# Kernel optimization log

Hardware: AMD Instinct MI355X
Metric: run time of the kernel (lower is better)

Reference implementation:

```python
import jax, jax.numpy as jnp
import numpy as np

N_NODES = 200000
N_EDGES = 6400000
IN_FEAT = 128
HIDDEN = 16


def gcn_conv(x, W, b, row, col, n):
    # PyG GCNConv: h = X W ; out_i = sum_{(j->i)} d_j^{-1/2} d_i^{-1/2} h_j + b
    # (row = source j, col = target i; self-loops already included in row/col)
    deg = jax.ops.segment_sum(jnp.ones_like(col, dtype=x.dtype), col, num_segments=n)
    dinv = jnp.where(deg > 0, jax.lax.rsqrt(deg), jnp.zeros_like(deg))
    norm = dinv[row] * dinv[col]            # [E+N]
    h = x @ W                               # [N, out] small GEMM
    msg = norm[:, None] * h[row]            # gather over edges
    out = jax.ops.segment_sum(msg, col, num_segments=n)  # scatter-add to targets
    return out + b


def setup_inputs() -> dict:
    key = jax.random.key(0)
    k1, k2, k3, k4 = jax.random.split(key, 4)
    x = jax.random.normal(k1, (N_NODES, IN_FEAT), dtype=jnp.float32)
    edge_index = jax.random.randint(k2, (2, N_EDGES), 0, N_NODES, dtype=jnp.int32)
    # Glorot-ish init for the two linear layers
    W1 = jax.random.normal(k3, (IN_FEAT, HIDDEN), dtype=jnp.float32) / np.sqrt(IN_FEAT)
    W2 = jax.random.normal(k4, (HIDDEN, 1), dtype=jnp.float32) / np.sqrt(HIDDEN)
    b1 = jnp.zeros((HIDDEN,), dtype=jnp.float32)
    b2 = jnp.zeros((1,), dtype=jnp.float32)
    return {"x": x, "edge_index": edge_index, "W1": W1, "b1": b1, "W2": W2, "b2": b2}


def reference(x, edge_index, W1, b1, W2, b2):
    n = x.shape[0]
    # add self-loops (as PyG GCNConv does by default)
    loop = jnp.arange(n, dtype=edge_index.dtype)
    row = jnp.concatenate([edge_index[0], loop])
    col = jnp.concatenate([edge_index[1], loop])
    h = gcn_conv(x, W1, b1, row, col, n)    # [N, 16]
    h = jax.nn.relu(h)
    out = gcn_conv(h, W2, b2, row, col, n)  # [N, 1]
    return out.squeeze(-1)                  # [N]
```

## Files before the change

kernel.cpp:

```cpp
#include <hip/hip_runtime.h>
#include <hip/hip_fp16.h>

#define N_NODES 200000
#define N_EDGES 6400000
#define IN_FEAT 128
#define HIDDEN  16

#define RN 128
#define NRF 1568
#define NC 98
#define CSHIFT 11
#define NPAD (NRF * RN)
#define SRC_MASK 0x3FFFFu
#define SB1 8192
#define SB2 8192
#define BPB 9
#define CAP 5120

typedef float v4f __attribute__((ext_vector_type(4)));
typedef _Float16 f16x8 __attribute__((ext_vector_type(8)));
typedef float f32x4 __attribute__((ext_vector_type(4)));


__global__ __launch_bounds__(256) void k_fcnt(const int* __restrict__ col,
                                              unsigned* __restrict__ fcnt) {
    __shared__ unsigned c[NRF];
    for (int i = threadIdx.x; i < NRF; i += 256) c[i] = 0u;
    __syncthreads();
    const int EPB = N_EDGES / 512;
    const int4* c4 = (const int4*)(col + (size_t)blockIdx.x * EPB);
    for (int i = threadIdx.x; i < EPB / 4; i += 256) {
        int4 v = c4[i];
        atomicAdd(&c[(unsigned)v.x >> 7], 1u);
        atomicAdd(&c[(unsigned)v.y >> 7], 1u);
        atomicAdd(&c[(unsigned)v.z >> 7], 1u);
        atomicAdd(&c[(unsigned)v.w >> 7], 1u);
    }
    __syncthreads();
    for (int i = threadIdx.x; i < NRF; i += 256)
        if (c[i]) atomicAdd(&fcnt[i], c[i]);
}


__global__ __launch_bounds__(1024) void k_scanr(const unsigned* __restrict__ fcnt,
                                                unsigned* __restrict__ foffs,
                                                unsigned* __restrict__ fcur,
                                                unsigned* __restrict__ coffs,
                                                unsigned* __restrict__ ccur) {
    __shared__ unsigned s[1024];
    const int t = threadIdx.x;
    unsigned c0 = (2 * t     < NRF) ? fcnt[2 * t]     : 0u;
    unsigned c1 = (2 * t + 1 < NRF) ? fcnt[2 * t + 1] : 0u;
    unsigned pairsum = c0 + c1;
    s[t] = pairsum;
    __syncthreads();
    #pragma unroll
    for (int d = 1; d < 1024; d <<= 1) {
        unsigned add = (t >= d) ? s[t - d] : 0u;
        __syncthreads();
        s[t] += add;
        __syncthreads();
    }
    unsigned excl = s[t] - pairsum;
    if (2 * t < NRF)     { foffs[2 * t]     = excl;      fcur[2 * t]     = excl; }
    if (2 * t + 1 < NRF) { foffs[2 * t + 1] = excl + c0; fcur[2 * t + 1] = excl + c0; }
    if (t == 1023) foffs[NRF] = s[t];
    __syncthreads();
    if (t < NC)  { unsigned v = foffs[16 * t]; coffs[t] = v; ccur[t] = v; }
    if (t == NC) coffs[NC] = N_EDGES;
}


__global__ __launch_bounds__(256) void k_cscat(const int* __restrict__ row,
                                               const int* __restrict__ col,
                                               unsigned* __restrict__ ccur,
                                               unsigned* __restrict__ tmp1) {
    __shared__ unsigned cnt[NC], gbase[NC], lcur[NC];
    const long long e0 = (long long)blockIdx.x * SB1;
    long long rem = (long long)N_EDGES - e0;
    const int n = rem > SB1 ? SB1 : (int)rem;
    if (threadIdx.x < NC) { cnt[threadIdx.x] = 0u; lcur[threadIdx.x] = 0u; }
    __syncthreads();
    const int4* c4 = (const int4*)(col + e0);
    for (int i = threadIdx.x; i < n / 4; i += 256) {
        int4 v = c4[i];
        atomicAdd(&cnt[(unsigned)v.x >> CSHIFT], 1u);
        atomicAdd(&cnt[(unsigned)v.y >> CSHIFT], 1u);
        atomicAdd(&cnt[(unsigned)v.z >> CSHIFT], 1u);
        atomicAdd(&cnt[(unsigned)v.w >> CSHIFT], 1u);
    }
    __syncthreads();
    if (threadIdx.x < NC)
        gbase[threadIdx.x] = cnt[threadIdx.x] ? atomicAdd(&ccur[threadIdx.x], cnt[threadIdx.x]) : 0u;
    __syncthreads();
    for (int i = threadIdx.x; i < n; i += 256) {
        unsigned c = (unsigned)col[e0 + i];
        unsigned s = (unsigned)row[e0 + i];
        unsigned b = c >> CSHIFT;
        unsigned pos = gbase[b] + atomicAdd(&lcur[b], 1u);
        tmp1[pos] = ((c & 2047u) << 18) | s;
    }
}


__global__ __launch_bounds__(256) void k_fscat(const unsigned* __restrict__ tmp1,
                                               const unsigned* __restrict__ coffs,
                                               unsigned* __restrict__ fcur,
                                               unsigned* __restrict__ tmp2) {
    __shared__ unsigned cnt[16], gbase[16], lcur[16];
    const int b = blockIdx.x / BPB;
    const int sl = blockIdx.x % BPB;
    const unsigned blo = coffs[b], bhi = coffs[b + 1];
    const unsigned lo = blo + (unsigned)sl * SB2;
    if (lo >= bhi) return;
    const unsigned hi = (lo + SB2 < bhi) ? lo + SB2 : bhi;
    const unsigned n = hi - lo;
    if (threadIdx.x < 16) { cnt[threadIdx.x] = 0u; lcur[threadIdx.x] = 0u; }
    __syncthreads();
    for (unsigned i = threadIdx.x; i < n; i += 256)
        atomicAdd(&cnt[tmp1[lo + i] >> 25], 1u);
    __syncthreads();
    if (threadIdx.x < 16)
        gbase[threadIdx.x] = cnt[threadIdx.x]
            ? atomicAdd(&fcur[16 * b + threadIdx.x], cnt[threadIdx.x]) : 0u;
    __syncthreads();
    for (unsigned i = threadIdx.x; i < n; i += 256) {
        unsigned p = tmp1[lo + i];
        unsigned f = p >> 25;
        unsigned pos = gbase[f] + atomicAdd(&lcur[f], 1u);
        tmp2[pos] = p & 0x01FFFFFFu;
    }
}


__global__ __launch_bounds__(256) void k_bsort(const unsigned* __restrict__ tmp,
                                               const unsigned* __restrict__ boffs_r,
                                               unsigned* __restrict__ boffs_n,
                                               float* __restrict__ dinv,
                                               unsigned* __restrict__ sorted) {
    __shared__ unsigned ebuf[CAP];
    __shared__ unsigned obuf[CAP];
    __shared__ unsigned dcnt[RN], dcur[RN], sscan[RN];
    const int r = blockIdx.x;
    const unsigned lo = boffs_r[r], hi = boffs_r[r + 1];
    const unsigned cnt = hi - lo;
    const unsigned node0 = (unsigned)r * RN;
    if (threadIdx.x < RN) dcnt[threadIdx.x] = 0u;
    __syncthreads();

    const bool fits = (cnt <= CAP);
    if (fits) {
        for (unsigned i = threadIdx.x; i < cnt; i += 256) {
            unsigned p = tmp[lo + i];
            ebuf[i] = p;
            atomicAdd(&dcnt[p >> 18], 1u);
        }
    } else {
        for (unsigned i = threadIdx.x; i < cnt; i += 256)
            atomicAdd(&dcnt[tmp[lo + i] >> 18], 1u);
    }
    __syncthreads();

    unsigned c = 0;
    if (threadIdx.x < RN) { c = dcnt[threadIdx.x]; sscan[threadIdx.x] = c; }
    __syncthreads();
    #pragma unroll
    for (int d = 1; d < RN; d <<= 1) {
        unsigned add = 0;
        if (threadIdx.x < RN && threadIdx.x >= d) add = sscan[threadIdx.x - d];
        __syncthreads();
        if (threadIdx.x < RN) sscan[threadIdx.x] += add;
        __syncthreads();
    }
    if (threadIdx.x < RN) {
        unsigned excl = sscan[threadIdx.x] - c;
        dcur[threadIdx.x] = excl;
        unsigned node = node0 + threadIdx.x;
        boffs_n[node] = lo + excl;
        if (node < N_NODES) dinv[node] = rsqrtf((float)c + 1.0f);
    }
    if (r == NRF - 1 && threadIdx.x == 0) boffs_n[NPAD] = hi;
    __syncthreads();

    if (fits) {
        for (unsigned i = threadIdx.x; i < cnt; i += 256) {
            unsigned p = ebuf[i];
            unsigned pos = atomicAdd(&dcur[p >> 18], 1u);
            obuf[pos] = p & SRC_MASK;
        }
        __syncthreads();
        for (unsigned i = threadIdx.x; i < cnt; i += 256)
            sorted[lo + i] = obuf[i];
    } else {
        for (unsigned i = threadIdx.x; i < cnt; i += 256) {
            unsigned p = tmp[lo + i];
            unsigned pos = atomicAdd(&dcur[p >> 18], 1u);
            sorted[lo + pos] = p & SRC_MASK;
        }
    }
}


__global__ __launch_bounds__(256) void k_gemm1(const float* __restrict__ x,
                                               const float* __restrict__ W1,
                                               const float* __restrict__ dinv,
                                               __half* __restrict__ h16) {
    const int wave = (blockIdx.x * 256 + threadIdx.x) >> 6;
    const int lane = threadIdx.x & 63;
    const int m16 = lane & 15;
    const int quad = lane >> 4;
    if (wave * 16 >= N_NODES) return;

    f16x8 bf[4];
    #pragma unroll
    for (int kb = 0; kb < 4; ++kb)
        #pragma unroll
        for (int j = 0; j < 8; ++j)
            bf[kb][j] = (_Float16)W1[(kb * 32 + quad * 8 + j) * HIDDEN + m16];

    const int node0 = wave * 16;
    const float* xrow = x + (size_t)(node0 + m16) * IN_FEAT + quad * 8;
    f32x4 acc = {0.f, 0.f, 0.f, 0.f};
    #pragma unroll
    for (int kb = 0; kb < 4; ++kb) {
        const v4f* p = (const v4f*)(xrow + kb * 32);
        v4f u0 = p[0], u1 = p[1];
        f16x8 af;
        af[0] = (_Float16)u0.x; af[1] = (_Float16)u0.y;
        af[2] = (_Float16)u0.z; af[3] = (_Float16)u0.w;
        af[4] = (_Float16)u1.x; af[5] = (_Float16)u1.y;
        af[6] = (_Float16)u1.z; af[7] = (_Float16)u1.w;
        acc = __builtin_amdgcn_mfma_f32_16x16x32_f16(af, bf[kb], acc, 0, 0, 0);
    }
    #pragma unroll
    for (int r = 0; r < 4; ++r) {
        int node = node0 + quad * 4 + r;
        h16[(size_t)node * HIDDEN + m16] = __float2half(dinv[node] * acc[r]);
    }
}


__global__ __launch_bounds__(256) void k_agg1(const unsigned* __restrict__ sorted,
                                              const unsigned* __restrict__ boffs,
                                              const unsigned* __restrict__ h16u,
                                              const float* __restrict__ dinv,
                                              const float* __restrict__ b1,
                                              const float* __restrict__ W2,
                                              float* __restrict__ tp) {
    const unsigned tid = blockIdx.x * 256 + threadIdx.x;
    const unsigned node = tid >> 3;
    const int l = tid & 7;
    if (node >= N_NODES) return;

    unsigned e = boffs[node];
    const unsigned o1 = boffs[node + 1];
    float ax = 0.f, ay = 0.f;

    unsigned n0 = 0, n1 = 0, n2 = 0, n3 = 0;
    bool have = (e + 4 <= o1);
    if (have) { n0 = sorted[e]; n1 = sorted[e + 1]; n2 = sorted[e + 2]; n3 = sorted[e + 3]; }
    while (have) {
        unsigned c0 = n0, c1 = n1, c2 = n2, c3 = n3;
        e += 4;
        have = (e + 4 <= o1);
        if (have) { n0 = sorted[e]; n1 = sorted[e + 1]; n2 = sorted[e + 2]; n3 = sorted[e + 3]; }
        unsigned v0 = h16u[(size_t)c0 * 8 + l];
        unsigned v1 = h16u[(size_t)c1 * 8 + l];
        unsigned v2 = h16u[(size_t)c2 * 8 + l];
        unsigned v3 = h16u[(size_t)c3 * 8 + l];
        float2 f0 = __half22float2(*(const __half2*)&v0);
        float2 f1 = __half22float2(*(const __half2*)&v1);
        float2 f2 = __half22float2(*(const __half2*)&v2);
        float2 f3 = __half22float2(*(const __half2*)&v3);
        ax += f0.x + f1.x; ay += f0.y + f1.y;
        ax += f2.x + f3.x; ay += f2.y + f3.y;
    }
    for (; e < o1; ++e) {
        unsigned s = sorted[e];
        unsigned v = h16u[(size_t)s * 8 + l];
        float2 f = __half22float2(*(const __half2*)&v);
        ax += f.x; ay += f.y;
    }

    unsigned vs = h16u[(size_t)node * 8 + l];
    float2 fs = __half22float2(*(const __half2*)&vs);
    float di = dinv[node];
    float px = fmaf(di, ax + fs.x, b1[2 * l]);
    float py = fmaf(di, ay + fs.y, b1[2 * l + 1]);
    float r = fmaxf(px, 0.f) * W2[2 * l] + fmaxf(py, 0.f) * W2[2 * l + 1];
    r += __shfl_xor(r, 4, 8);
    r += __shfl_xor(r, 2, 8);
    r += __shfl_xor(r, 1, 8);
    if (l == 0) tp[node] = di * r;
}


__global__ __launch_bounds__(256) void k_agg2(const unsigned* __restrict__ sorted,
                                              const unsigned* __restrict__ boffs,
                                              const float* __restrict__ tp,
                                              const float* __restrict__ dinv,
                                              const float* __restrict__ b2,
                                              float* __restrict__ out) {
    const unsigned node = blockIdx.x * 256 + threadIdx.x;
    if (node >= N_NODES) return;

    unsigned e = boffs[node];
    const unsigned o1 = boffs[node + 1];
    float acc = 0.f;

    unsigned n0 = 0, n1 = 0, n2 = 0, n3 = 0;
    bool have = (e + 4 <= o1);
    if (have) { n0 = sorted[e]; n1 = sorted[e + 1]; n2 = sorted[e + 2]; n3 = sorted[e + 3]; }
    while (have) {
        unsigned c0 = n0, c1 = n1, c2 = n2, c3 = n3;
        e += 4;
        have = (e + 4 <= o1);
        if (have) { n0 = sorted[e]; n1 = sorted[e + 1]; n2 = sorted[e + 2]; n3 = sorted[e + 3]; }
        float t0 = tp[c0];
        float t1 = tp[c1];
        float t2 = tp[c2];
        float t3 = tp[c3];
        acc += t0 + t1;
        acc += t2 + t3;
    }
    for (; e < o1; ++e) acc += tp[sorted[e]];

    out[node] = fmaf(dinv[node], tp[node] + acc, b2[0]);
}


extern "C" void kernel_launch(void* const* d_in, const int* in_sizes, int n_in,
                              void* d_out, int out_size, void* d_ws, size_t ws_size,
                              hipStream_t stream) {
    const float* x   = (const float*)d_in[0];
    const int*   ei  = (const int*)d_in[1];
    const float* W1  = (const float*)d_in[2];
    const float* b1  = (const float*)d_in[3];
    const float* W2  = (const float*)d_in[4];
    const float* b2  = (const float*)d_in[5];
    float* out = (float*)d_out;

    const int* row = ei;
    const int* col = ei + N_EDGES;

    unsigned* fcnt    = (unsigned*)d_ws;
    unsigned* foffs   = fcnt + 2048;
    unsigned* fcur    = foffs + 2048;
    unsigned* coffs   = fcur + 2048;
    unsigned* ccur    = coffs + 128;
    unsigned* boffs_n = ccur + 128;
    float*    dinv    = (float*)(boffs_n + NPAD + 64);
    float*    tp      = dinv + N_NODES;
    __half*   h16     = (__half*)(tp + N_NODES);
    unsigned* tmp1    = (unsigned*)(h16 + (size_t)N_NODES * HIDDEN);
    unsigned* tmp2    = tmp1 + N_EDGES;
    unsigned* sorted  = tmp1;

    (void)hipMemsetAsync(fcnt, 0, 2048 * sizeof(unsigned), stream);
    k_fcnt<<<512, 256, 0, stream>>>(col, fcnt);
    k_scanr<<<1, 1024, 0, stream>>>(fcnt, foffs, fcur, coffs, ccur);
    k_cscat<<<(N_EDGES + SB1 - 1) / SB1, 256, 0, stream>>>(row, col, ccur, tmp1);
    k_fscat<<<NC * BPB, 256, 0, stream>>>(tmp1, coffs, fcur, tmp2);
    k_bsort<<<NRF, 256, 0, stream>>>(tmp2, foffs, boffs_n, dinv, sorted);
    k_gemm1<<<(N_NODES / 16 + 3) / 4, 256, 0, stream>>>(x, W1, dinv, h16);
    k_agg1<<<(N_NODES * 8) / 256 + 1, 256, 0, stream>>>(sorted, boffs_n, (const unsigned*)h16,
                                                        dinv, b1, W2, tp);
    k_agg2<<<(N_NODES + 255) / 256, 256, 0, stream>>>(sorted, boffs_n, tp, dinv, b2, out);
}
```

Measured before the change: 443.0 us.

## Widen sort blocks, vectorize cscat scatter, drop bsort staging, unroll aggregation by eight

Raises the block size of the three binning kernels to 512 threads. k_cscat now reads row and col as int4 in its scatter loop. k_bsort drops its shared staging buffer and reads tmp from global memory twice, which frees LDS for occupancy. Both aggregation kernels deepen their gather unroll from 4 to 8 to keep more loads in flight, at the cost of more registers and a longer scalar tail for low-degree nodes.

```diff
diff --git a/kernel.cpp b/kernel.cpp
--- a/kernel.cpp
+++ b/kernel.cpp
@@ -22,14 +22,14 @@
 typedef float f32x4 __attribute__((ext_vector_type(4)));
 
 
-__global__ __launch_bounds__(256) void k_fcnt(const int* __restrict__ col,
+__global__ __launch_bounds__(512) void k_fcnt(const int* __restrict__ col,
                                               unsigned* __restrict__ fcnt) {
     __shared__ unsigned c[NRF];
-    for (int i = threadIdx.x; i < NRF; i += 256) c[i] = 0u;
+    for (int i = threadIdx.x; i < NRF; i += 512) c[i] = 0u;
     __syncthreads();
     const int EPB = N_EDGES / 512;
     const int4* c4 = (const int4*)(col + (size_t)blockIdx.x * EPB);
-    for (int i = threadIdx.x; i < EPB / 4; i += 256) {
+    for (int i = threadIdx.x; i < EPB / 4; i += 512) {
         int4 v = c4[i];
         atomicAdd(&c[(unsigned)v.x >> 7], 1u);
         atomicAdd(&c[(unsigned)v.y >> 7], 1u);
@@ -37,7 +37,7 @@
         atomicAdd(&c[(unsigned)v.w >> 7], 1u);
     }
     __syncthreads();
-    for (int i = threadIdx.x; i < NRF; i += 256)
+    for (int i = threadIdx.x; i < NRF; i += 512)
         if (c[i]) atomicAdd(&fcnt[i], c[i]);
 }
 
@@ -71,7 +71,7 @@
 }
 
 
-__global__ __launch_bounds__(256) void k_cscat(const int* __restrict__ row,
+__global__ __launch_bounds__(512) void k_cscat(const int* __restrict__ row,
                                                const int* __restrict__ col,
                                                unsigned* __restrict__ ccur,
                                                unsigned* __restrict__ tmp1) {
@@ -82,7 +82,8 @@
     if (threadIdx.x < NC) { cnt[threadIdx.x] = 0u; lcur[threadIdx.x] = 0u; }
     __syncthreads();
     const int4* c4 = (const int4*)(col + e0);
-    for (int i = threadIdx.x; i < n / 4; i += 256) {
+    const int4* r4 = (const int4*)(row + e0);
+    for (int i = threadIdx.x; i < n / 4; i += 512) {
         int4 v = c4[i];
         atomicAdd(&cnt[(unsigned)v.x >> CSHIFT], 1u);
         atomicAdd(&cnt[(unsigned)v.y >> CSHIFT], 1u);
@@ -93,17 +94,23 @@
     if (threadIdx.x < NC)
         gbase[threadIdx.x] = cnt[threadIdx.x] ? atomicAdd(&ccur[threadIdx.x], cnt[threadIdx.x]) : 0u;
     __syncthreads();
-    for (int i = threadIdx.x; i < n; i += 256) {
-        unsigned c = (unsigned)col[e0 + i];
-        unsigned s = (unsigned)row[e0 + i];
-        unsigned b = c >> CSHIFT;
-        unsigned pos = gbase[b] + atomicAdd(&lcur[b], 1u);
-        tmp1[pos] = ((c & 2047u) << 18) | s;
-    }
-}
-
-
-__global__ __launch_bounds__(256) void k_fscat(const unsigned* __restrict__ tmp1,
+    for (int i = threadIdx.x; i < n / 4; i += 512) {
+        int4 c = c4[i];
+        int4 r = r4[i];
+        unsigned b, pos;
+        b = (unsigned)c.x >> CSHIFT; pos = gbase[b] + atomicAdd(&lcur[b], 1u);
+        tmp1[pos] = (((unsigned)c.x & 2047u) << 18) | (unsigned)r.x;
+        b = (unsigned)c.y >> CSHIFT; pos = gbase[b] + atomicAdd(&lcur[b], 1u);
+        tmp1[pos] = (((unsigned)c.y & 2047u) << 18) | (unsigned)r.y;
+        b = (unsigned)c.z >> CSHIFT; pos = gbase[b] + atomicAdd(&lcur[b], 1u);
+        tmp1[pos] = (((unsigned)c.z & 2047u) << 18) | (unsigned)r.z;
+        b = (unsigned)c.w >> CSHIFT; pos = gbase[b] + atomicAdd(&lcur[b], 1u);
+        tmp1[pos] = (((unsigned)c.w & 2047u) << 18) | (unsigned)r.w;
+    }
+}
+
+
+__global__ __launch_bounds__(512) void k_fscat(const unsigned* __restrict__ tmp1,
                                                const unsigned* __restrict__ coffs,
                                                unsigned* __restrict__ fcur,
                                                unsigned* __restrict__ tmp2) {
@@ -117,14 +124,14 @@
     const unsigned n = hi - lo;
     if (threadIdx.x < 16) { cnt[threadIdx.x] = 0u; lcur[threadIdx.x] = 0u; }
     __syncthreads();
-    for (unsigned i = threadIdx.x; i < n; i += 256)
+    for (unsigned i = threadIdx.x; i < n; i += 512)
         atomicAdd(&cnt[tmp1[lo + i] >> 25], 1u);
     __syncthreads();
     if (threadIdx.x < 16)
         gbase[threadIdx.x] = cnt[threadIdx.x]
             ? atomicAdd(&fcur[16 * b + threadIdx.x], cnt[threadIdx.x]) : 0u;
     __syncthreads();
-    for (unsigned i = threadIdx.x; i < n; i += 256) {
+    for (unsigned i = threadIdx.x; i < n; i += 512) {
         unsigned p = tmp1[lo + i];
         unsigned f = p >> 25;
         unsigned pos = gbase[f] + atomicAdd(&lcur[f], 1u);
@@ -138,7 +145,6 @@
                                                unsigned* __restrict__ boffs_n,
                                                float* __restrict__ dinv,
                                                unsigned* __restrict__ sorted) {
-    __shared__ unsigned ebuf[CAP];
     __shared__ unsigned obuf[CAP];
     __shared__ unsigned dcnt[RN], dcur[RN], sscan[RN];
     const int r = blockIdx.x;
@@ -148,17 +154,8 @@
     if (threadIdx.x < RN) dcnt[threadIdx.x] = 0u;
     __syncthreads();
 
-    const bool fits = (cnt <= CAP);
-    if (fits) {
-        for (unsigned i = threadIdx.x; i < cnt; i += 256) {
-            unsigned p = tmp[lo + i];
-            ebuf[i] = p;
-            atomicAdd(&dcnt[p >> 18], 1u);
-        }
-    } else {
-        for (unsigned i = threadIdx.x; i < cnt; i += 256)
-            atomicAdd(&dcnt[tmp[lo + i] >> 18], 1u);
-    }
+    for (unsigned i = threadIdx.x; i < cnt; i += 256)
+        atomicAdd(&dcnt[tmp[lo + i] >> 18], 1u);
     __syncthreads();
 
     unsigned c = 0;
@@ -182,9 +179,9 @@
     if (r == NRF - 1 && threadIdx.x == 0) boffs_n[NPAD] = hi;
     __syncthreads();
 
-    if (fits) {
+    if (cnt <= CAP) {
         for (unsigned i = threadIdx.x; i < cnt; i += 256) {
-            unsigned p = ebuf[i];
+            unsigned p = tmp[lo + i];
             unsigned pos = atomicAdd(&dcur[p >> 18], 1u);
             obuf[pos] = p & SRC_MASK;
         }
@@ -256,24 +253,40 @@
     const unsigned o1 = boffs[node + 1];
     float ax = 0.f, ay = 0.f;
 
-    unsigned n0 = 0, n1 = 0, n2 = 0, n3 = 0;
-    bool have = (e + 4 <= o1);
-    if (have) { n0 = sorted[e]; n1 = sorted[e + 1]; n2 = sorted[e + 2]; n3 = sorted[e + 3]; }
+    unsigned n0, n1, n2, n3, n4, n5, n6, n7;
+    bool have = (e + 8 <= o1);
+    if (have) {
+        n0 = sorted[e];     n1 = sorted[e + 1]; n2 = sorted[e + 2]; n3 = sorted[e + 3];
+        n4 = sorted[e + 4]; n5 = sorted[e + 5]; n6 = sorted[e + 6]; n7 = sorted[e + 7];
+    }
     while (have) {
-        unsigned c0 = n0, c1 = n1, c2 = n2, c3 = n3;
-        e += 4;
-        have = (e + 4 <= o1);
-        if (have) { n0 = sorted[e]; n1 = sorted[e + 1]; n2 = sorted[e + 2]; n3 = sorted[e + 3]; }
+        unsigned c0 = n0, c1 = n1, c2 = n2, c3 = n3, c4 = n4, c5 = n5, c6 = n6, c7 = n7;
+        e += 8;
+        have = (e + 8 <= o1);
+        if (have) {
+            n0 = sorted[e];     n1 = sorted[e + 1]; n2 = sorted[e + 2]; n3 = sorted[e + 3];
+            n4 = sorted[e + 4]; n5 = sorted[e + 5]; n6 = sorted[e + 6]; n7 = sorted[e + 7];
+        }
         unsigned v0 = h16u[(size_t)c0 * 8 + l];
         unsigned v1 = h16u[(size_t)c1 * 8 + l];
         unsigned v2 = h16u[(size_t)c2 * 8 + l];
         unsigned v3 = h16u[(size_t)c3 * 8 + l];
+        unsigned v4 = h16u[(size_t)c4 * 8 + l];
+        unsigned v5 = h16u[(size_t)c5 * 8 + l];
+        unsigned v6 = h16u[(size_t)c6 * 8 + l];
+        unsigned v7 = h16u[(size_t)c7 * 8 + l];
         float2 f0 = __half22float2(*(const __half2*)&v0);
         float2 f1 = __half22float2(*(const __half2*)&v1);
         float2 f2 = __half22float2(*(const __half2*)&v2);
         float2 f3 = __half22float2(*(const __half2*)&v3);
-        ax += f0.x + f1.x; ay += f0.y + f1.y;
-        ax += f2.x + f3.x; ay += f2.y + f3.y;
+        float2 f4 = __half22float2(*(const __half2*)&v4);
+        float2 f5 = __half22float2(*(const __half2*)&v5);
+        float2 f6 = __half22float2(*(const __half2*)&v6);
+        float2 f7 = __half22float2(*(const __half2*)&v7);
+        ax += f0.x + f1.x + f2.x + f3.x;
+        ay += f0.y + f1.y + f2.y + f3.y;
+        ax += f4.x + f5.x + f6.x + f7.x;
+        ay += f4.y + f5.y + f6.y + f7.y;
     }
     for (; e < o1; ++e) {
         unsigned s = sorted[e];
@@ -308,20 +321,24 @@
     const unsigned o1 = boffs[node + 1];
     float acc = 0.f;
 
-    unsigned n0 = 0, n1 = 0, n2 = 0, n3 = 0;
-    bool have = (e + 4 <= o1);
-    if (have) { n0 = sorted[e]; n1 = sorted[e + 1]; n2 = sorted[e + 2]; n3 = sorted[e + 3]; }
+    unsigned n0, n1, n2, n3, n4, n5, n6, n7;
+    bool have = (e + 8 <= o1);
+    if (have) {
+        n0 = sorted[e];     n1 = sorted[e + 1]; n2 = sorted[e + 2]; n3 = sorted[e + 3];
+        n4 = sorted[e + 4]; n5 = sorted[e + 5]; n6 = sorted[e + 6]; n7 = sorted[e + 7];
+    }
     while (have) {
-        unsigned c0 = n0, c1 = n1, c2 = n2, c3 = n3;
-        e += 4;
-        have = (e + 4 <= o1);
-        if (have) { n0 = sorted[e]; n1 = sorted[e + 1]; n2 = sorted[e + 2]; n3 = sorted[e + 3]; }
-        float t0 = tp[c0];
-        float t1 = tp[c1];
-        float t2 = tp[c2];
-        float t3 = tp[c3];
-        acc += t0 + t1;
-        acc += t2 + t3;
+        unsigned c0 = n0, c1 = n1, c2 = n2, c3 = n3, c4 = n4, c5 = n5, c6 = n6, c7 = n7;
+        e += 8;
+        have = (e + 8 <= o1);
+        if (have) {
+            n0 = sorted[e];     n1 = sorted[e + 1]; n2 = sorted[e + 2]; n3 = sorted[e + 3];
+            n4 = sorted[e + 4]; n5 = sorted[e + 5]; n6 = sorted[e + 6]; n7 = sorted[e + 7];
+        }
+        float t0 = tp[c0], t1 = tp[c1], t2 = tp[c2], t3 = tp[c3];
+        float t4 = tp[c4], t5 = tp[c5], t6 = tp[c6], t7 = tp[c7];
+        acc += t0 + t1 + t2 + t3;
+        acc += t4 + t5 + t6 + t7;
     }
     for (; e < o1; ++e) acc += tp[sorted[e]];
 
@@ -357,10 +374,10 @@
     unsigned* sorted  = tmp1;
 
     (void)hipMemsetAsync(fcnt, 0, 2048 * sizeof(unsigned), stream);
-    k_fcnt<<<512, 256, 0, stream>>>(col, fcnt);
+    k_fcnt<<<512, 512, 0, stream>>>(col, fcnt);
     k_scanr<<<1, 1024, 0, stream>>>(fcnt, foffs, fcur, coffs, ccur);
-    k_cscat<<<(N_EDGES + SB1 - 1) / SB1, 256, 0, stream>>>(row, col, ccur, tmp1);
-    k_fscat<<<NC * BPB, 256, 0, stream>>>(tmp1, coffs, fcur, tmp2);
+    k_cscat<<<(N_EDGES + SB1 - 1) / SB1, 512, 0, stream>>>(row, col, ccur, tmp1);
+    k_fscat<<<NC * BPB, 512, 0, stream>>>(tmp1, coffs, fcur, tmp2);
     k_bsort<<<NRF, 256, 0, stream>>>(tmp2, foffs, boffs_n, dinv, sorted);
     k_gemm1<<<(N_NODES / 16 + 3) / 4, 256, 0, stream>>>(x, W1, dinv, h16);
     k_agg1<<<(N_NODES * 8) / 256 + 1, 256, 0, stream>>>(sorted, boffs_n, (const unsigned*)h16,
```

Measured after the change: 409.8 us. -7.5%, faster.
